# Performance work log

Measured on AMD Instinct MI355X. Metric: run time of the kernel, lower is better.

Reference implementation:

```python
import jax, jax.numpy as jnp
import numpy as np

B = 2
D = 256          # d_model == q_model
NH = 8           # heads
DH = D // NH
NP = 4           # sampling points per level
LV = 4           # feature levels
NQ = 4096        # queries
NL = 6           # encoder layers
DFF = 1024
SHAPES = [(128, 128), (64, 64), (32, 32), (16, 16)]
S = sum(h * w for h, w in SHAPES)


def setup_inputs() -> dict:
    key = jax.random.key(0)
    ks = iter(jax.random.split(key, 64))
    d = {}
    for l, (h, w) in enumerate(SHAPES):
        d[f"src{l}"] = jax.random.normal(next(ks), (B, D, h, w), jnp.float32)
        d[f"pos{l}"] = jax.random.normal(next(ks), (B, D, h, w), jnp.float32)
        d[f"mask{l}"] = jnp.zeros((B, h, w), jnp.bool_)
    d["q_feat"] = jax.random.normal(next(ks), (B, NQ, D), jnp.float32)
    d["q_pos"] = jax.random.normal(next(ks), (B, NQ, D), jnp.float32)
    d["q_ref"] = jax.random.uniform(next(ks), (B, NQ, 2), jnp.float32)
    d["level_embed"] = jax.random.normal(next(ks), (LV, D), jnp.float32) * 0.02

    def p(shape):
        return jax.random.normal(next(ks), shape, jnp.float32) * 0.02

    d["so_w"] = p((NL, NH * LV * NP * 2, D)); d["so_b"] = p((NL, NH * LV * NP * 2))
    d["aw_w"] = p((NL, NH * LV * NP, D));     d["aw_b"] = p((NL, NH * LV * NP))
    d["vp_w"] = p((NL, D, D)); d["vp_b"] = p((NL, D))
    d["op_w"] = p((NL, D, D)); d["op_b"] = p((NL, D))
    d["n1_g"] = jnp.ones((NL, D)); d["n1_b"] = jnp.zeros((NL, D))
    d["l1_w"] = p((NL, DFF, D)); d["l1_b"] = p((NL, DFF))
    d["l2_w"] = p((NL, D, DFF)); d["l2_b"] = p((NL, D))
    d["n2_g"] = jnp.ones((NL, D)); d["n2_b"] = jnp.zeros((NL, D))
    return d


def _ln(x, g, b):
    m = x.mean(-1, keepdims=True)
    v = ((x - m) ** 2).mean(-1, keepdims=True)
    return (x - m) * jax.lax.rsqrt(v + 1e-5) * g + b


def _bilinear(v, loc, Hl, Wl):
    # v: [B,NH,Hl*Wl,DH], loc: [B,NH,NQ,NP,2] normalized to [0,1]
    # grid_sample semantics, align_corners=False, zero padding
    x = loc[..., 0] * Wl - 0.5
    y = loc[..., 1] * Hl - 0.5
    x0 = jnp.floor(x); y0 = jnp.floor(y)
    wx = x - x0; wy = y - y0
    out = jnp.zeros((B, NH, NQ, NP, DH), v.dtype)
    for dx, dy in ((0, 0), (1, 0), (0, 1), (1, 1)):
        xc = x0 + dx; yc = y0 + dy
        w = (wx if dx else 1.0 - wx) * (wy if dy else 1.0 - wy)
        valid = (xc >= 0) & (xc < Wl) & (yc >= 0) & (yc < Hl)
        xi = jnp.clip(xc, 0, Wl - 1).astype(jnp.int32)
        yi = jnp.clip(yc, 0, Hl - 1).astype(jnp.int32)
        idx = (yi * Wl + xi).reshape(B, NH, NQ * NP)
        g = jnp.take_along_axis(v, idx[..., None], axis=2).reshape(B, NH, NQ, NP, DH)
        out = out + g * (w * valid)[..., None]
    return out


def _msda(q, ref, value, pad_mask, so_w, so_b, aw_w, aw_b, vp_w, vp_b, op_w, op_b):
    # q: [B,NQ,D]; ref: [B,NQ,LV,2]; value: [B,S,D]; pad_mask: [B,S] bool
    v = jnp.einsum('bsd,ed->bse', value, vp_w) + vp_b
    v = jnp.where(pad_mask[..., None], 0.0, v)
    v = v.reshape(B, S, NH, DH).transpose(0, 2, 1, 3)  # [B,NH,S,DH]
    offs = (jnp.einsum('bqd,od->bqo', q, so_w) + so_b).reshape(B, NQ, NH, LV, NP, 2)
    aw = (jnp.einsum('bqd,od->bqo', q, aw_w) + aw_b).reshape(B, NQ, NH, LV * NP)
    aw = jax.nn.softmax(aw, axis=-1).reshape(B, NQ, NH, LV, NP)
    norm = jnp.array([[w, h] for h, w in SHAPES], jnp.float32)  # (W,H) per level
    loc = ref[:, :, None, :, None, :] + offs / norm[None, None, None, :, None, :]
    loc = loc.transpose(0, 2, 1, 3, 4, 5)  # [B,NH,NQ,LV,NP,2]
    start = 0
    samp = []
    for l, (Hl, Wl) in enumerate(SHAPES):
        vl = v[:, :, start:start + Hl * Wl]
        start += Hl * Wl
        samp.append(_bilinear(vl, loc[:, :, :, l], Hl, Wl))
    samp = jnp.stack(samp, axis=3)  # [B,NH,NQ,LV,NP,DH]
    out = jnp.einsum('bhqlpd,bqhlp->bqhd', samp, aw).reshape(B, NQ, D)
    return jnp.einsum('bqd,od->bqo', out, op_w) + op_b


def _forward(srcs, poss, masks, q_feat, q_pos, q_ref, level_embed,
             so_w, so_b, aw_w, aw_b, vp_w, vp_b, op_w, op_b,
             n1_g, n1_b, l1_w, l1_b, l2_w, l2_b, n2_g, n2_b):
    src_flat, mask_flat = [], []
    for lvl, (s, m, p) in enumerate(zip(srcs, masks, poss)):
        b, c, h, w = s.shape
        src_flat.append(s.reshape(b, c, h * w).transpose(0, 2, 1))
        mask_flat.append(m.reshape(b, h * w))
        # lvl_pos_embed = p + level_embed[lvl]  (computed in torch but unused by layers)
    src_flat = jnp.concatenate(src_flat, axis=1)   # [B,S,D]
    mask_flat = jnp.concatenate(mask_flat, axis=1)  # [B,S]
    vrs = []
    for m in masks:
        _, H, W = m.shape
        vH = jnp.sum(~m[:, :, 0], axis=1).astype(jnp.float32) / H
        vW = jnp.sum(~m[:, 0, :], axis=1).astype(jnp.float32) / W
        vrs.append(jnp.stack([vW, vH], axis=-1))
    valid_ratios = jnp.stack(vrs, axis=1)  # [B,LV,2]
    ref = q_ref[:, :, None, :] * valid_ratios[:, None]  # [B,NQ,LV,2]
    qf = q_feat
    for l in range(NL):
        src2 = _msda(qf + q_pos, ref, src_flat, mask_flat,
                     so_w[l], so_b[l], aw_w[l], aw_b[l],
                     vp_w[l], vp_b[l], op_w[l], op_b[l])
        qf = _ln(qf + src2, n1_g[l], n1_b[l])
        h = jax.nn.relu(jnp.einsum('bqd,fd->bqf', qf, l1_w[l]) + l1_b[l])
        ff = jnp.einsum('bqf,df->bqd', h, l2_w[l]) + l2_b[l]
        qf = _ln(qf + ff, n2_g[l], n2_b[l])
    return qf


def reference(src0, src1, src2, src3, pos0, pos1, pos2, pos3,
              mask0, mask1, mask2, mask3, q_feat, q_pos, q_ref, level_embed,
              so_w, so_b, aw_w, aw_b, vp_w, vp_b, op_w, op_b,
              n1_g, n1_b, l1_w, l1_b, l2_w, l2_b, n2_g, n2_b):
    return _forward([src0, src1, src2, src3], [pos0, pos1, pos2, pos3],
                    [mask0, mask1, mask2, mask3], q_feat, q_pos, q_ref, level_embed,
                    so_w, so_b, aw_w, aw_b, vp_w, vp_b, op_w, op_b,
                    n1_g, n1_b, l1_w, l1_b, l2_w, l2_b, n2_g, n2_b)
```

## Files before the change

kernel.cpp:

```cpp
#include <hip/hip_runtime.h>
#include <math.h>

#define BB 2
#define DD 256
#define NH 8
#define DH 32
#define NPNP 4
#define LV 4
#define NQ 4096
#define NL 6
#define DFF 1024
#define SS 21760

typedef short v8s __attribute__((ext_vector_type(8)));
typedef float v4f __attribute__((ext_vector_type(4)));

__device__ __forceinline__ ushort f2b(float f) {
    union { float f; unsigned u; } v; v.f = f;
    unsigned r = v.u + 0x7fffu + ((v.u >> 16) & 1u);
    return (ushort)(r >> 16);
}

__device__ __constant__ int c_dims[4]   = {128, 64, 32, 16};
__device__ __constant__ int c_starts[4] = {0, 16384, 20480, 21504};
__device__ __constant__ int c_hw[4]     = {16384, 4096, 1024, 256};

__global__ __launch_bounds__(256) void flatten_all_kernel(
    const float* __restrict__ s0p, const float* __restrict__ s1p,
    const float* __restrict__ s2p, const float* __restrict__ s3p,
    ushort* __restrict__ dst)
{
    __shared__ float tile[64][65];
    int bx = blockIdx.x;
    int l, ls;
    if (bx < 256)      { l = 0; ls = bx; }
    else if (bx < 320) { l = 1; ls = bx - 256; }
    else if (bx < 336) { l = 2; ls = bx - 320; }
    else               { l = 3; ls = bx - 336; }
    const float* srcs[4] = {s0p, s1p, s2p, s3p};
    const float* src = srcs[l];
    const int HW = c_hw[l];
    const int start = c_starts[l];
    const int b  = blockIdx.z;
    const int d0 = blockIdx.y * 64;
    const int s0 = ls * 64;
    const int t  = threadIdx.x;
    const float* sp = src + ((size_t)b * DD + d0) * (size_t)HW + s0;
#pragma unroll
    for (int i = 0; i < 16; ++i) {
        int lin = i * 256 + t;
        int dl = lin >> 6, sl = lin & 63;
        tile[sl][dl] = sp[(size_t)dl * HW + sl];
    }
    __syncthreads();
    ushort* dp = dst + ((size_t)b * SS + start + s0) * DD + d0;
#pragma unroll
    for (int i = 0; i < 16; ++i) {
        int lin = i * 256 + t;
        int sl = lin >> 6, dl = lin & 63;
        dp[(size_t)sl * DD + dl] = f2b(tile[sl][dl]);
    }
}

__global__ __launch_bounds__(256) void cvt_all_kernel(
    const float* __restrict__ so, const float* __restrict__ aw,
    const float* __restrict__ vp, const float* __restrict__ op,
    const float* __restrict__ l1, const float* __restrict__ l2,
    ushort* __restrict__ qso, ushort* __restrict__ qaw,
    ushort* __restrict__ qvp, ushort* __restrict__ qop,
    ushort* __restrict__ ql1, ushort* __restrict__ ql2)
{
    int i = blockIdx.x * 256 + threadIdx.x;
    const float* in; ushort* out; int j;
    if (i < 98304)       { in = so; out = qso; j = i; }
    else if (i < 147456) { in = aw; out = qaw; j = i - 98304; }
    else if (i < 245760) { in = vp; out = qvp; j = i - 147456; }
    else if (i < 344064) { in = op; out = qop; j = i - 245760; }
    else if (i < 737280) { in = l1; out = ql1; j = i - 344064; }
    else                 { in = l2; out = ql2; j = i - 737280; }
    float4 x = ((const float4*)in)[j];
    uint2 pk;
    pk.x = (unsigned)f2b(x.x) | ((unsigned)f2b(x.y) << 16);
    pk.y = (unsigned)f2b(x.z) | ((unsigned)f2b(x.w) << 16);
    ((uint2*)out)[j] = pk;
}

__global__ __launch_bounds__(256) void add_bf_kernel(
    const float* __restrict__ a, const float* __restrict__ b,
    ushort* __restrict__ o, int n4)
{
    int i = blockIdx.x * 256 + threadIdx.x;
    if (i < n4) {
        float4 x = ((const float4*)a)[i];
        float4 y = ((const float4*)b)[i];
        uint2 pk;
        pk.x = (unsigned)f2b(x.x + y.x) | ((unsigned)f2b(x.y + y.y) << 16);
        pk.y = (unsigned)f2b(x.z + y.z) | ((unsigned)f2b(x.w + y.w) << 16);
        ((uint2*)o)[i] = pk;
    }
}

__global__ __launch_bounds__(256) void vp_gemm_kernel(
    const ushort* __restrict__ A, const ushort* __restrict__ W,
    const float* __restrict__ bias, ushort* __restrict__ out)
{
    __shared__ ushort As[128 * 64];
    __shared__ ushort Ws[128 * 64];
    const int tid  = threadIdx.x;
    const int wave = tid >> 6, lane = tid & 63;

    const int lin = blockIdx.x;
    const int s   = lin / 48;
    const int w48 = lin - s * 48;
    const int z   = w48 >> 3;
    const int t   = s * 8 + (w48 & 7);
    const int rb  = t % 340;
    const int eb  = t / 340;
    const size_t r0 = (size_t)rb * 128;
    const int e0 = eb * 128;
    const int wrow = wave >> 1, wcol = wave & 1;
    const ushort* Wz = W + (size_t)z * 65536;

    v4f acc[4][4];
#pragma unroll
    for (int m = 0; m < 4; ++m)
#pragma unroll
        for (int n = 0; n < 4; ++n)
#pragma unroll
            for (int j = 0; j < 4; ++j) acc[m][n][j] = 0.f;

    const int srow   = lane >> 3;
    const int schunk = (lane & 7) ^ (srow & 7);
    const ushort* Ag = A + (r0 + wave * 8 + srow) * 256 + schunk * 8;
    const ushort* Wg = Wz + ((size_t)(e0 + wave * 8 + srow)) * 256 + schunk * 8;

    for (int k0 = 0; k0 < 256; k0 += 64) {
#pragma unroll
        for (int i = 0; i < 4; ++i) {
            __builtin_amdgcn_global_load_lds(
                (const __attribute__((address_space(1))) void*)(Ag + (size_t)(i * 32) * 256 + k0),
                (__attribute__((address_space(3))) void*)(As + (i * 32 + wave * 8) * 64),
                16, 0, 0);
            __builtin_amdgcn_global_load_lds(
                (const __attribute__((address_space(1))) void*)(Wg + (size_t)(i * 32) * 256 + k0),
                (__attribute__((address_space(3))) void*)(Ws + (i * 32 + wave * 8) * 64),
                16, 0, 0);
        }
        __syncthreads();

        const int rlo = lane & 15;
#pragma unroll
        for (int ks = 0; ks < 2; ++ks) {
            const int chi = ks * 4 + (lane >> 4);
            v8s af[4], bf[4];
#pragma unroll
            for (int m = 0; m < 4; ++m) {
                int r = wrow * 64 + m * 16 + rlo;
                af[m] = *(const v8s*)((const char*)As + r * 128 + ((chi ^ (r & 7)) << 4));
            }
#pragma unroll
            for (int n = 0; n < 4; ++n) {
                int r = wcol * 64 + n * 16 + rlo;
                bf[n] = *(const v8s*)((const char*)Ws + r * 128 + ((chi ^ (r & 7)) << 4));
            }
#pragma unroll
            for (int m = 0; m < 4; ++m)
#pragma unroll
                for (int n = 0; n < 4; ++n)
                    acc[m][n] = __builtin_amdgcn_mfma_f32_16x16x32_bf16(
                        af[m], bf[n], acc[m][n], 0, 0, 0);
        }
        __syncthreads();
    }

    const int lrow = (lane >> 4) << 2;
    const int lcol = lane & 15;
    ushort* oz = out + (size_t)z * BB * SS * 256;
#pragma unroll
    for (int m = 0; m < 4; ++m) {
#pragma unroll
        for (int n = 0; n < 4; ++n) {
            const int ecol = e0 + wcol * 64 + n * 16 + lcol;
            const float bv = bias[z * 256 + ecol];
#pragma unroll
            for (int j = 0; j < 4; ++j) {
                const size_t row = r0 + wrow * 64 + m * 16 + lrow + j;
                oz[row * 256 + ecol] = f2b(acc[m][n][j] + bv);
            }
        }
    }
}

enum { EPI_RELUB = 1, EPI_QF = 4 };

template <int K, int EPI, int MF>
__global__ __launch_bounds__(256) void gemm_bf16(
    const ushort* __restrict__ A, const ushort* __restrict__ W,
    const float* __restrict__ bias, void* __restrict__ out, int E,
    const ushort* __restrict__ W2, const float* __restrict__ bias2,
    void* __restrict__ out2)
{
    __shared__ ushort As[MF * 32 * 64];
    __shared__ ushort Ws[128 * 64];
    const int tid  = threadIdx.x;
    const int wave = tid >> 6, lane = tid & 63;
    const size_t r0 = (size_t)blockIdx.x * (MF * 32);
    const int e0 = blockIdx.y * 128;
    const int wrow = wave >> 1, wcol = wave & 1;

    const ushort* Wbase = W;
    const float*  bbase = bias;
    int eoff = 0;
    if (EPI == EPI_QF && blockIdx.y == 2) {
        Wbase = W2; bbase = bias2; eoff = 256;
    }

    v4f acc[MF][4];
#pragma unroll
    for (int m = 0; m < MF; ++m)
#pragma unroll
        for (int n = 0; n < 4; ++n)
#pragma unroll
            for (int j = 0; j < 4; ++j) acc[m][n][j] = 0.f;

    const int srow   = lane >> 3;
    const int schunk = (lane & 7) ^ (srow & 7);
    const ushort* Ag = A + (r0 + wave * 8 + srow) * K + schunk * 8;
    const ushort* Wg = Wbase + ((size_t)(e0 - eoff + wave * 8 + srow)) * K + schunk * 8;

    for (int k0 = 0; k0 < K; k0 += 64) {
#pragma unroll
        for (int i = 0; i < MF; ++i) {
            __builtin_amdgcn_global_load_lds(
                (const __attribute__((address_space(1))) void*)(Ag + (size_t)(i * 32) * K + k0),
                (__attribute__((address_space(3))) void*)(As + (i * 32 + wave * 8) * 64),
                16, 0, 0);
        }
#pragma unroll
        for (int i = 0; i < 4; ++i) {
            __builtin_amdgcn_global_load_lds(
                (const __attribute__((address_space(1))) void*)(Wg + (size_t)(i * 32) * K + k0),
                (__attribute__((address_space(3))) void*)(Ws + (i * 32 + wave * 8) * 64),
                16, 0, 0);
        }
        __syncthreads();

        const int rlo = lane & 15;
#pragma unroll
        for (int ks = 0; ks < 2; ++ks) {
            const int chi = ks * 4 + (lane >> 4);
            v8s af[MF], bf[4];
#pragma unroll
            for (int m = 0; m < MF; ++m) {
                int r = wrow * (MF * 16) + m * 16 + rlo;
                af[m] = *(const v8s*)((const char*)As + r * 128 + ((chi ^ (r & 7)) << 4));
            }
#pragma unroll
            for (int n = 0; n < 4; ++n) {
                int r = wcol * 64 + n * 16 + rlo;
                bf[n] = *(const v8s*)((const char*)Ws + r * 128 + ((chi ^ (r & 7)) << 4));
            }
#pragma unroll
            for (int m = 0; m < MF; ++m)
#pragma unroll
                for (int n = 0; n < 4; ++n)
                    acc[m][n] = __builtin_amdgcn_mfma_f32_16x16x32_bf16(
                        af[m], bf[n], acc[m][n], 0, 0, 0);
        }
        __syncthreads();
    }

    const int lrow = (lane >> 4) << 2;
    const int lcol = lane & 15;
#pragma unroll
    for (int m = 0; m < MF; ++m) {
#pragma unroll
        for (int n = 0; n < 4; ++n) {
            const int ecol = e0 + wcol * 64 + n * 16 + lcol;
            const float bv = bbase[ecol - eoff];
#pragma unroll
            for (int j = 0; j < 4; ++j) {
                const size_t row = r0 + wrow * (MF * 16) + m * 16 + lrow + j;
                float val = acc[m][n][j] + bv;
                if (EPI == EPI_RELUB) {
                    ((ushort*)out)[row * E + ecol] = f2b(fmaxf(val, 0.f));
                } else {
                    if (eoff == 0) ((float*)out)[row * 256 + ecol] = val;
                    else           ((float*)out2)[row * 128 + (ecol - 256)] = val;
                }
            }
        }
    }
}

template <int K, bool ADDPOS>
__global__ __launch_bounds__(256) void gemm_ln_kernel(
    const ushort* __restrict__ A, const ushort* __restrict__ W,
    const float* __restrict__ bias, const float* __restrict__ res,
    const float* __restrict__ g, const float* __restrict__ beta,
    float* __restrict__ outF, ushort* __restrict__ outB,
    const float* __restrict__ pos)
{
    __shared__ ushort As[32 * 64];
    __shared__ ushort Ws[256 * 64];
    __shared__ float rsum[2][32], rsq[2][32];
    const int tid  = threadIdx.x;
    const int wave = tid >> 6, lane = tid & 63;
    const size_t r0 = (size_t)blockIdx.x * 32;
    const int wrow = wave >> 1, wcol = wave & 1;
    const int rlo = lane & 15;

    v4f acc[8];
#pragma unroll
    for (int n = 0; n < 8; ++n)
#pragma unroll
        for (int j = 0; j < 4; ++j) acc[n][j] = 0.f;

    const int arow = tid >> 3;
    const int asc  = (tid & 7) ^ (arow & 7);

    for (int k0 = 0; k0 < K; k0 += 64) {
        __builtin_amdgcn_global_load_lds(
            (const __attribute__((address_space(1))) void*)(A + (r0 + arow) * K + k0 + asc * 8),
            (__attribute__((address_space(3))) void*)(As + (size_t)tid * 8),
            16, 0, 0);
#pragma unroll
        for (int i = 0; i < 8; ++i) {
            int lin = i * 256 + tid;
            int wr = lin >> 3;
            int wsc = (lin & 7) ^ (wr & 7);
            __builtin_amdgcn_global_load_lds(
                (const __attribute__((address_space(1))) void*)(W + (size_t)wr * K + k0 + wsc * 8),
                (__attribute__((address_space(3))) void*)(Ws + (size_t)lin * 8),
                16, 0, 0);
        }
        __syncthreads();
#pragma unroll
        for (int ks = 0; ks < 2; ++ks) {
            const int chi = ks * 4 + (lane >> 4);
            const int ra = wrow * 16 + rlo;
            v8s af = *(const v8s*)((const char*)As + ra * 128 + ((chi ^ (ra & 7)) << 4));
            v8s bf[8];
#pragma unroll
            for (int n = 0; n < 8; ++n) {
                int rb = wcol * 128 + n * 16 + rlo;
                bf[n] = *(const v8s*)((const char*)Ws + rb * 128 + ((chi ^ (rb & 7)) << 4));
            }
#pragma unroll
            for (int n = 0; n < 8; ++n)
                acc[n] = __builtin_amdgcn_mfma_f32_16x16x32_bf16(af, bf[n], acc[n], 0, 0, 0);
        }
        __syncthreads();
    }

    const int lrow = (lane >> 4) << 2;
    const int lcol = lane & 15;
    float sums[4] = {0.f, 0.f, 0.f, 0.f};
    float sqs[4]  = {0.f, 0.f, 0.f, 0.f};
#pragma unroll
    for (int n = 0; n < 8; ++n) {
        const int ecol = wcol * 128 + n * 16 + lcol;
        const float bv = bias[ecol];
#pragma unroll
        for (int j = 0; j < 4; ++j) {
            const size_t row = r0 + wrow * 16 + lrow + j;
            float v = acc[n][j] + bv + res[row * 256 + ecol];
            acc[n][j] = v;
            sums[j] += v;
            sqs[j]  += v * v;
        }
    }
#pragma unroll
    for (int off = 1; off < 16; off <<= 1) {
#pragma unroll
        for (int j = 0; j < 4; ++j) {
            sums[j] += __shfl_xor(sums[j], off);
            sqs[j]  += __shfl_xor(sqs[j], off);
        }
    }
    if ((lane & 15) == 0) {
#pragma unroll
        for (int j = 0; j < 4; ++j) {
            int ridx = wrow * 16 + lrow + j;
            rsum[wcol][ridx] = sums[j];
            rsq[wcol][ridx]  = sqs[j];
        }
    }
    __syncthreads();
#pragma unroll
    for (int j = 0; j < 4; ++j) {
        const int ridx = wrow * 16 + lrow + j;
        const float s  = rsum[0][ridx] + rsum[1][ridx];
        const float sq = rsq[0][ridx] + rsq[1][ridx];
        const float mean = s * (1.f / 256.f);
        const float var  = sq * (1.f / 256.f) - mean * mean;
        const float rstd = rsqrtf(var + 1e-5f);
        const size_t row = r0 + wrow * 16 + lrow + j;
#pragma unroll
        for (int n = 0; n < 8; ++n) {
            const int ecol = wcol * 128 + n * 16 + lcol;
            float o = (acc[n][j] - mean) * rstd * g[ecol] + beta[ecol];
            outF[row * 256 + ecol] = o;
            float ob = ADDPOS ? (o + pos[row * 256 + ecol]) : o;
            outB[row * 256 + ecol] = f2b(ob);
        }
    }
}

__global__ __launch_bounds__(256) void msda_kernel(
    const ushort* __restrict__ v, const float* __restrict__ offs,
    const float* __restrict__ awb, const float* __restrict__ qref,
    ushort* __restrict__ out)
{
    __shared__ uint2 iw[4][128][4];
    const int wid  = threadIdx.x >> 6;
    const int lane = threadIdx.x & 63;
    const int gid  = blockIdx.x * 4 + wid;
    const int q = gid & (NQ - 1);
    const int b = gid >> 12;
    const size_t bq = (size_t)b * NQ + q;

    const float rx = qref[bq * 2 + 0];
    const float ry = qref[bq * 2 + 1];

#pragma unroll
    for (int it = 0; it < 2; ++it) {
        const int t = it * 64 + lane;
        const int pp = t & 15;
        const int lvl = pp >> 2;
        float a_raw = awb[bq * 128 + t];
        float mx = a_raw;
        mx = fmaxf(mx, __shfl_xor(mx, 1));
        mx = fmaxf(mx, __shfl_xor(mx, 2));
        mx = fmaxf(mx, __shfl_xor(mx, 4));
        mx = fmaxf(mx, __shfl_xor(mx, 8));
        float e = expf(a_raw - mx);
        float sum = e;
        sum += __shfl_xor(sum, 1);
        sum += __shfl_xor(sum, 2);
        sum += __shfl_xor(sum, 4);
        sum += __shfl_xor(sum, 8);
        const float a = e / sum;

        float2 oxy = *(const float2*)(offs + bq * 256 + t * 2);
        const int Wl = c_dims[lvl];
        const int st = c_starts[lvl];
        const float fW = (float)Wl;
        float x = fmaf(rx, fW, oxy.x) - 0.5f;
        float y = fmaf(ry, fW, oxy.y) - 0.5f;
        float x0f = floorf(x), y0f = floorf(y);
        float wx = x - x0f, wy = y - y0f;
        int x0 = (int)x0f, y0 = (int)y0f;
        const unsigned hoff = (unsigned)((t >> 4) * 64);
#pragma unroll
        for (int c = 0; c < 4; ++c) {
            int dx = c & 1, dy = c >> 1;
            int xc = x0 + dx, yc = y0 + dy;
            bool valid = (xc >= 0) & (xc < Wl) & (yc >= 0) & (yc < Wl);
            int xi = min(max(xc, 0), Wl - 1);
            int yi = min(max(yc, 0), Wl - 1);
            float w = (dx ? wx : 1.f - wx) * (dy ? wy : 1.f - wy);
            uint2 tt;
            tt.x = (unsigned)((st + yi * Wl + xi) * 512) + hoff;
            tt.y = __float_as_uint(valid ? a * w : 0.f);
            iw[wid][t][c] = tt;
        }
    }
    __syncthreads();

    const int c   = lane >> 4;
    const int dh2 = lane & 15;
    const char* vbase = (const char*)(v + (size_t)b * SS * 256) + dh2 * 4;
#pragma unroll
    for (int h = 0; h < NH; ++h) {
        float acc0 = 0.f, acc1 = 0.f;
#pragma unroll
        for (int p = 0; p < 16; ++p) {
            uint2 t = iw[wid][h * 16 + p][c];
            float cw = __uint_as_float(t.y);
            unsigned v2 = *(const unsigned*)(vbase + t.x);
            float lo = __uint_as_float(v2 << 16);
            float hi = __uint_as_float(v2 & 0xffff0000u);
            acc0 = fmaf(cw, lo, acc0);
            acc1 = fmaf(cw, hi, acc1);
        }
        acc0 += __shfl_xor(acc0, 16); acc0 += __shfl_xor(acc0, 32);
        acc1 += __shfl_xor(acc1, 16); acc1 += __shfl_xor(acc1, 32);
        if (lane < 16) {
            unsigned pk = (unsigned)f2b(acc0) | ((unsigned)f2b(acc1) << 16);
            *(unsigned*)(out + bq * DD + h * DH + dh2 * 2) = pk;
        }
    }
}

extern "C" void kernel_launch(void* const* d_in, const int* in_sizes, int n_in,
                              void* d_out, int out_size, void* d_ws, size_t ws_size,
                              hipStream_t stream)
{
    const float* src[4]  = {(const float*)d_in[0], (const float*)d_in[3],
                            (const float*)d_in[6], (const float*)d_in[9]};
    const float* q_feat  = (const float*)d_in[12];
    const float* q_pos   = (const float*)d_in[13];
    const float* q_ref   = (const float*)d_in[14];
    const float* so_w = (const float*)d_in[16];
    const float* so_b = (const float*)d_in[17];
    const float* aw_w = (const float*)d_in[18];
    const float* aw_b = (const float*)d_in[19];
    const float* vp_w = (const float*)d_in[20];
    const float* vp_b = (const float*)d_in[21];
    const float* op_w = (const float*)d_in[22];
    const float* op_b = (const float*)d_in[23];
    const float* n1_g = (const float*)d_in[24];
    const float* n1_b = (const float*)d_in[25];
    const float* l1_w = (const float*)d_in[26];
    const float* l1_b = (const float*)d_in[27];
    const float* l2_w = (const float*)d_in[28];
    const float* l2_b = (const float*)d_in[29];
    const float* n2_g = (const float*)d_in[30];
    const float* n2_b = (const float*)d_in[31];

    char* p = (char*)d_ws;
    auto alloc = [&](size_t bytes) { char* r = p; p += (bytes + 255) & ~255ULL; return r; };

    ushort* src_flat = (ushort*)alloc((size_t)BB * SS * DD * 2);
    ushort* v_buf6   = (ushort*)alloc((size_t)NL * BB * SS * DD * 2);
    ushort* q_bf     = (ushort*)alloc((size_t)BB * NQ * DD * 2);
    float*  offs     = (float*) alloc((size_t)BB * NQ * 256 * 4);
    float*  awb      = (float*) alloc((size_t)BB * NQ * 128 * 4);
    ushort* msda_bf  = (ushort*)alloc((size_t)BB * NQ * DD * 2);
    ushort* hbuf     = (ushort*)alloc((size_t)BB * NQ * DFF * 2);
    ushort* qf_bf    = (ushort*)alloc((size_t)BB * NQ * DD * 2);
    ushort* w_so     = (ushort*)alloc((size_t)NL * 256 * 256 * 2);
    ushort* w_aw     = (ushort*)alloc((size_t)NL * 128 * 256 * 2);
    ushort* w_vp     = (ushort*)alloc((size_t)NL * 256 * 256 * 2);
    ushort* w_op     = (ushort*)alloc((size_t)NL * 256 * 256 * 2);
    ushort* w_l1     = (ushort*)alloc((size_t)NL * DFF * 256 * 2);
    ushort* w_l2     = (ushort*)alloc((size_t)NL * 256 * DFF * 2);

    float* qf = (float*)d_out;

    cvt_all_kernel<<<4416, 256, 0, stream>>>(
        so_w, aw_w, vp_w, op_w, l1_w, l2_w,
        w_so, w_aw, w_vp, w_op, w_l1, w_l2);

    flatten_all_kernel<<<dim3(340, 4, 2), 256, 0, stream>>>(
        src[0], src[1], src[2], src[3], src_flat);

    const int RQ = BB * NQ;
    const int RV = BB * SS;

    add_bf_kernel<<<RQ * DD / (256 * 4), 256, 0, stream>>>(q_feat, q_pos, q_bf, RQ * DD / 4);

    vp_gemm_kernel<<<4080, 256, 0, stream>>>(
        src_flat, w_vp, vp_b, v_buf6);

    for (int l = 0; l < NL; ++l) {
        gemm_bf16<256, EPI_QF, 2><<<dim3(RQ / 64, 3), 256, 0, stream>>>(
            q_bf, w_so + (size_t)l * 256 * 256, so_b + (size_t)l * 256, offs, 256,
            w_aw + (size_t)l * 128 * 256, aw_b + (size_t)l * 128, awb);

        msda_kernel<<<(BB * NQ) / 4, 256, 0, stream>>>(
            v_buf6 + (size_t)l * BB * SS * DD, offs, awb, q_ref, msda_bf);

        gemm_ln_kernel<256, false><<<RQ / 32, 256, 0, stream>>>(
            msda_bf, w_op + (size_t)l * 256 * 256, op_b + (size_t)l * 256,
            (l == 0 ? q_feat : qf), n1_g + l * 256, n1_b + l * 256,
            qf, qf_bf, nullptr);

        gemm_bf16<256, EPI_RELUB, 4><<<dim3(RQ / 128, DFF / 128), 256, 0, stream>>>(
            qf_bf, w_l1 + (size_t)l * DFF * 256, l1_b + (size_t)l * DFF, hbuf, DFF,
            nullptr, nullptr, nullptr);

        gemm_ln_kernel<1024, true><<<RQ / 32, 256, 0, stream>>>(
            hbuf, w_l2 + (size_t)l * 256 * DFF, l2_b + (size_t)l * 256,
            qf, n2_g + l * 256, n2_b + l * 256,
            qf, q_bf, q_pos);
    }

    (void)in_sizes; (void)n_in; (void)out_size; (void)ws_size;
}
```

Baseline: 538.8 us.

## Fuse output projection+LayerNorm with FFN first linear layer in one kernel

Adds a kernel that computes the output projection, residual add and LayerNorm for 32 rows, keeps the normalized bf16 rows in shared memory, then loops over DFF in 128-column chunks to compute the ReLU first FFN layer. This drops the qf_bf round trip through global memory and one kernel launch per layer. In exchange each block streams the full l1 weight through one shared buffer with little overlap, only 256 blocks launch for the FFN GEMM instead of 512, and shared memory per block rises, which may reduce occupancy.

```diff
diff --git a/kernel.cpp b/kernel.cpp
--- a/kernel.cpp
+++ b/kernel.cpp
@@ -288,6 +288,172 @@
                     if (eoff == 0) ((float*)out)[row * 256 + ecol] = val;
                     else           ((float*)out2)[row * 128 + (ecol - 256)] = val;
                 }
+            }
+        }
+    }
+}
+
+__global__ __launch_bounds__(256) void opln_l1_kernel(
+    const ushort* __restrict__ A,  const ushort* __restrict__ Wop,
+    const float* __restrict__ bop, const float* __restrict__ res,
+    const float* __restrict__ g,   const float* __restrict__ beta,
+    const ushort* __restrict__ Wl1, const float* __restrict__ bl1,
+    float* __restrict__ outF, ushort* __restrict__ hbuf)
+{
+    __shared__ ushort As[32 * 64];
+    __shared__ ushort Ws[256 * 64];
+    __shared__ ushort Aln[32 * 256];
+    __shared__ float rsum[2][32], rsq[2][32];
+    const int tid  = threadIdx.x;
+    const int wave = tid >> 6, lane = tid & 63;
+    const size_t r0 = (size_t)blockIdx.x * 32;
+    const int wrow = wave >> 1, wcol = wave & 1;
+    const int rlo = lane & 15;
+
+    v4f acc[8];
+#pragma unroll
+    for (int n = 0; n < 8; ++n)
+#pragma unroll
+        for (int j = 0; j < 4; ++j) acc[n][j] = 0.f;
+
+    const int arow = tid >> 3;
+    const int asc  = (tid & 7) ^ (arow & 7);
+
+    for (int k0 = 0; k0 < 256; k0 += 64) {
+        __builtin_amdgcn_global_load_lds(
+            (const __attribute__((address_space(1))) void*)(A + (r0 + arow) * 256 + k0 + asc * 8),
+            (__attribute__((address_space(3))) void*)(As + (size_t)tid * 8),
+            16, 0, 0);
+#pragma unroll
+        for (int i = 0; i < 8; ++i) {
+            int lin = i * 256 + tid;
+            int wr = lin >> 3;
+            int wsc = (lin & 7) ^ (wr & 7);
+            __builtin_amdgcn_global_load_lds(
+                (const __attribute__((address_space(1))) void*)(Wop + (size_t)wr * 256 + k0 + wsc * 8),
+                (__attribute__((address_space(3))) void*)(Ws + (size_t)lin * 8),
+                16, 0, 0);
+        }
+        __syncthreads();
+#pragma unroll
+        for (int ks = 0; ks < 2; ++ks) {
+            const int chi = ks * 4 + (lane >> 4);
+            const int ra = wrow * 16 + rlo;
+            v8s af = *(const v8s*)((const char*)As + ra * 128 + ((chi ^ (ra & 7)) << 4));
+            v8s bf[8];
+#pragma unroll
+            for (int n = 0; n < 8; ++n) {
+                int rb = wcol * 128 + n * 16 + rlo;
+                bf[n] = *(const v8s*)((const char*)Ws + rb * 128 + ((chi ^ (rb & 7)) << 4));
+            }
+#pragma unroll
+            for (int n = 0; n < 8; ++n)
+                acc[n] = __builtin_amdgcn_mfma_f32_16x16x32_bf16(af, bf[n], acc[n], 0, 0, 0);
+        }
+        __syncthreads();
+    }
+
+    const int lrow = (lane >> 4) << 2;
+    const int lcol = lane & 15;
+    float sums[4] = {0.f, 0.f, 0.f, 0.f};
+    float sqs[4]  = {0.f, 0.f, 0.f, 0.f};
+#pragma unroll
+    for (int n = 0; n < 8; ++n) {
+        const int ecol = wcol * 128 + n * 16 + lcol;
+        const float bv = bop[ecol];
+#pragma unroll
+        for (int j = 0; j < 4; ++j) {
+            const size_t row = r0 + wrow * 16 + lrow + j;
+            float v = acc[n][j] + bv + res[row * 256 + ecol];
+            acc[n][j] = v;
+            sums[j] += v;
+            sqs[j]  += v * v;
+        }
+    }
+#pragma unroll
+    for (int off = 1; off < 16; off <<= 1) {
+#pragma unroll
+        for (int j = 0; j < 4; ++j) {
+            sums[j] += __shfl_xor(sums[j], off);
+            sqs[j]  += __shfl_xor(sqs[j], off);
+        }
+    }
+    if ((lane & 15) == 0) {
+#pragma unroll
+        for (int j = 0; j < 4; ++j) {
+            int ridx = wrow * 16 + lrow + j;
+            rsum[wcol][ridx] = sums[j];
+            rsq[wcol][ridx]  = sqs[j];
+        }
+    }
+    __syncthreads();
+#pragma unroll
+    for (int j = 0; j < 4; ++j) {
+        const int ridx = wrow * 16 + lrow + j;
+        const float s  = rsum[0][ridx] + rsum[1][ridx];
+        const float sq = rsq[0][ridx] + rsq[1][ridx];
+        const float mean = s * (1.f / 256.f);
+        const float var  = sq * (1.f / 256.f) - mean * mean;
+        const float rstd = rsqrtf(var + 1e-5f);
+        const size_t row = r0 + ridx;
+#pragma unroll
+        for (int n = 0; n < 8; ++n) {
+            const int ecol = wcol * 128 + n * 16 + lcol;
+            float o = (acc[n][j] - mean) * rstd * g[ecol] + beta[ecol];
+            outF[row * 256 + ecol] = o;
+            const int rr = ridx;
+            Aln[rr * 256 + (((ecol >> 3) ^ (rr & 7)) << 3) + (ecol & 7)] = f2b(o);
+        }
+    }
+    __syncthreads();
+
+    for (int ec = 0; ec < 8; ++ec) {
+        v4f a2[4];
+#pragma unroll
+        for (int n = 0; n < 4; ++n)
+#pragma unroll
+            for (int j = 0; j < 4; ++j) a2[n][j] = 0.f;
+
+        for (int k0 = 0; k0 < 256; k0 += 64) {
+#pragma unroll
+            for (int i = 0; i < 4; ++i) {
+                int lin = i * 256 + tid;
+                int wr = lin >> 3;
+                int wsc = (lin & 7) ^ (wr & 7);
+                __builtin_amdgcn_global_load_lds(
+                    (const __attribute__((address_space(1))) void*)(
+                        Wl1 + (size_t)(ec * 128 + wr) * 256 + k0 + wsc * 8),
+                    (__attribute__((address_space(3))) void*)(Ws + (size_t)lin * 8),
+                    16, 0, 0);
+            }
+            __syncthreads();
+#pragma unroll
+            for (int ks = 0; ks < 2; ++ks) {
+                const int chiA = (k0 >> 3) + ks * 4 + (lane >> 4);
+                const int chiW = ks * 4 + (lane >> 4);
+                const int ra = wrow * 16 + rlo;
+                v8s af = *(const v8s*)((const char*)Aln + ra * 512 + ((chiA ^ (ra & 7)) << 4));
+                v8s bf[4];
+#pragma unroll
+                for (int n = 0; n < 4; ++n) {
+                    int rb = wcol * 64 + n * 16 + rlo;
+                    bf[n] = *(const v8s*)((const char*)Ws + rb * 128 + ((chiW ^ (rb & 7)) << 4));
+                }
+#pragma unroll
+                for (int n = 0; n < 4; ++n)
+                    a2[n] = __builtin_amdgcn_mfma_f32_16x16x32_bf16(af, bf[n], a2[n], 0, 0, 0);
+            }
+            __syncthreads();
+        }
+
+#pragma unroll
+        for (int n = 0; n < 4; ++n) {
+            const int col = ec * 128 + wcol * 64 + n * 16 + lcol;
+            const float bv = bl1[col];
+#pragma unroll
+            for (int j = 0; j < 4; ++j) {
+                const size_t row = r0 + wrow * 16 + lrow + j;
+                hbuf[row * DFF + col] = f2b(fmaxf(a2[n][j] + bv, 0.f));
             }
         }
     }
@@ -529,7 +695,6 @@
     float*  awb      = (float*) alloc((size_t)BB * NQ * 128 * 4);
     ushort* msda_bf  = (ushort*)alloc((size_t)BB * NQ * DD * 2);
     ushort* hbuf     = (ushort*)alloc((size_t)BB * NQ * DFF * 2);
-    ushort* qf_bf    = (ushort*)alloc((size_t)BB * NQ * DD * 2);
     ushort* w_so     = (ushort*)alloc((size_t)NL * 256 * 256 * 2);
     ushort* w_aw     = (ushort*)alloc((size_t)NL * 128 * 256 * 2);
     ushort* w_vp     = (ushort*)alloc((size_t)NL * 256 * 256 * 2);
@@ -562,14 +727,11 @@
         msda_kernel<<<(BB * NQ) / 4, 256, 0, stream>>>(
             v_buf6 + (size_t)l * BB * SS * DD, offs, awb, q_ref, msda_bf);
 
-        gemm_ln_kernel<256, false><<<RQ / 32, 256, 0, stream>>>(
+        opln_l1_kernel<<<RQ / 32, 256, 0, stream>>>(
             msda_bf, w_op + (size_t)l * 256 * 256, op_b + (size_t)l * 256,
             (l == 0 ? q_feat : qf), n1_g + l * 256, n1_b + l * 256,
-            qf, qf_bf, nullptr);
-
-        gemm_bf16<256, EPI_RELUB, 4><<<dim3(RQ / 128, DFF / 128), 256, 0, stream>>>(
-            qf_bf, w_l1 + (size_t)l * DFF * 256, l1_b + (size_t)l * DFF, hbuf, DFF,
-            nullptr, nullptr, nullptr);
+            w_l1 + (size_t)l * DFF * 256, l1_b + (size_t)l * DFF,
+            qf, hbuf);
 
         gemm_ln_kernel<1024, true><<<RQ / 32, 256, 0, stream>>>(
             hbuf, w_l2 + (size_t)l * 256 * DFF, l2_b + (size_t)l * 256,
```

After: 639.3 us. 1.19x slower.
